# Kernel tuning notes

Hardware: AMD Instinct MI355X
Metric: run time of the kernel (lower is better)

Reference implementation:

```python
import jax, jax.numpy as jnp
import numpy as np

B, N, K, D = 8, 4096, 16, 256


def layer_norm(x, g, b, eps=1e-5):
    m = jnp.mean(x, axis=-1, keepdims=True)
    v = jnp.var(x, axis=-1, keepdims=True)
    return (x - m) * jax.lax.rsqrt(v + eps) * g + b


def setup_inputs() -> dict:
    key = jax.random.key(0)
    ks = jax.random.split(key, 8)

    def lin(k, fi, fo):
        return (jax.random.normal(k, (fi, fo), jnp.float32) / np.sqrt(fi).astype(np.float32),
                jnp.zeros((fo,), jnp.float32))

    coordinates = jax.random.normal(ks[0], (B, N, 3), jnp.float32)
    W1, b1 = lin(ks[1], 10, D // 4)
    W2, b2 = lin(ks[2], D // 4, D // 2)
    W3, b3 = lin(ks[3], D // 2, D)
    Wa1, ba1 = lin(ks[4], D, D)
    Wa2, ba2 = lin(ks[5], D, D)
    return {
        'coordinates': coordinates,
        'W1': W1, 'b1': b1, 'g1': jnp.ones((D // 4,)), 'be1': jnp.zeros((D // 4,)),
        'W2': W2, 'b2': b2, 'g2': jnp.ones((D // 2,)), 'be2': jnp.zeros((D // 2,)),
        'W3': W3, 'b3': b3, 'g3': jnp.ones((D,)), 'be3': jnp.zeros((D,)),
        'Wa1': Wa1, 'ba1': ba1, 'ga1': jnp.ones((D,)), 'bea1': jnp.zeros((D,)),
        'Wa2': Wa2, 'ba2': ba2,
    }


def reference(coordinates, W1, b1, g1, be1, W2, b2, g2, be2, W3, b3, g3, be3,
              Wa1, ba1, ga1, bea1, Wa2, ba2):
    # kNN via squared-distance matrix (monotone in Euclidean distance)
    sq = jnp.sum(coordinates * coordinates, axis=-1)  # [B,N]
    d2 = sq[:, :, None] + sq[:, None, :] - 2.0 * jnp.einsum('bnd,bmd->bnm', coordinates, coordinates)
    _, idx = jax.lax.top_k(-d2, K)  # smallest K distances, [B,N,K]

    nbr = jax.vmap(lambda c, i: c[i])(coordinates, idx)  # [B,N,K,3]
    rel = nbr - coordinates[:, :, None, :]               # relative positions
    dist = jnp.linalg.norm(rel, axis=-1, keepdims=True)  # [B,N,K,1]
    rn = rel / (dist + 1e-6)
    axy = jnp.arctan2(rn[..., 1], rn[..., 0])[..., None]
    axz = jnp.arctan2(rn[..., 2], rn[..., 0])[..., None]
    ayz = jnp.arctan2(rn[..., 2], rn[..., 1])[..., None]
    geom = jnp.concatenate([dist, rel, axy, axz, ayz, rn], axis=-1)  # [B,N,K,10]

    # encoder MLP
    h = jax.nn.relu(layer_norm(geom @ W1 + b1, g1, be1))
    h = jax.nn.relu(layer_norm(h @ W2 + b2, g2, be2))
    h = layer_norm(h @ W3 + b3, g3, be3)

    agg = jnp.mean(h, axis=2)  # mean over neighbors -> [B,N,D]

    # aggregator MLP
    out = jax.nn.relu(layer_norm(agg @ Wa1 + ba1, ga1, bea1)) @ Wa2 + ba2
    return out
```

## Files before the change

kernel.cpp:

```cpp
#include <hip/hip_runtime.h>
#include <hip/hip_bf16.h>
#include <math.h>

#define BB 8
#define NN 4096
#define KK 16
#define DD 256

typedef __hip_bfloat16 bf16;
typedef _Float16 half8 __attribute__((ext_vector_type(8)));
typedef float f32x4 __attribute__((ext_vector_type(4)));

union HFU { _Float16 h; unsigned short u; };
__device__ __forceinline__ unsigned short f2h(float x) { HFU v; v.h = (_Float16)x; return v.u; }

#define CONV_TOTAL 273344
#define O_COORD 0
#define O_W1 98304
#define O_b1 98944
#define O_g1 99008
#define O_be1 99072
#define O_W2 99136
#define O_b2 107328
#define O_g2 107456
#define O_be2 107584
#define O_W3 107712
#define O_b3 140480
#define O_g3 140736
#define O_be3 140992
#define O_Wa1 141248
#define O_ba1 206784
#define O_ga1 207040
#define O_bea1 207296
#define O_Wa2 207552
#define O_ba2 273088

#define F_W1 0
#define F_W2 2048
#define F_W3 10240
#define F_A1 43008
#define F_A2 108544
#define FRAG_TOTAL 174080

struct SrcPtrs {
  const void* p[19];
};

__global__ __launch_bounds__(256) void convert_kernel(SrcPtrs sp, float* __restrict__ dst) {
  static constexpr int OFF[20] = {
      0,      98304,  98944,  99008,  99072,  99136,  107328, 107456, 107584,
      107712, 140480, 140736, 140992, 141248, 206784, 207040, 207296, 207552,
      273088, 273344};
  const int i = blockIdx.x * 256 + threadIdx.x;
  if (i >= CONV_TOTAL) return;
  const unsigned tag = ((const unsigned*)sp.p[3])[0];
  const bool isb = (tag == 0x3F803F80u);
  int s = 0;
#pragma unroll
  for (int j = 1; j < 19; j++)
    if (i >= OFF[j]) s = j;
  const int local = i - OFF[s];
  float v = isb ? __bfloat162float(((const bf16*)sp.p[s])[local])
                : ((const float*)sp.p[s])[local];
  dst[i] = v;
}

__global__ __launch_bounds__(256) void swizzle_kernel(const float* __restrict__ conv,
                                                      unsigned short* __restrict__ frag) {
  const int t = blockIdx.x * 256 + threadIdx.x;
  if (t >= FRAG_TOTAL) return;
  int l, e;
  if (t < 2048) { l = 0; e = t; }
  else if (t < 10240) { l = 1; e = t - 2048; }
  else if (t < 43008) { l = 2; e = t - 10240; }
  else if (t < 108544) { l = 3; e = t - 43008; }
  else { l = 4; e = t - 108544; }
  static constexpr int WOFF[5] = {O_W1, O_W2, O_W3, O_Wa1, O_Wa2};
  static constexpr int NDIM[5] = {64, 128, 256, 256, 256};
  static constexpr int NTC[5] = {4, 8, 16, 16, 16};
  static constexpr int KREAL[5] = {10, 64, 128, 256, 256};
  static constexpr int HOFF[5] = {F_W1, F_W2, F_W3, F_A1, F_A2};
  const int j = e & 7;
  const int lane = (e >> 3) & 63;
  const int tile = e >> 9;
  const int nt = tile % NTC[l];
  const int kt = tile / NTC[l];
  const int k = kt * 32 + (lane >> 4) * 8 + j;
  const int n = nt * 16 + (lane & 15);
  float w = (k < KREAL[l]) ? conv[WOFF[l] + k * NDIM[l] + n] : 0.0f;
  frag[HOFF[l] + e] = f2h(w);
}

__device__ __forceinline__ float sq3_rn(float x, float y, float z) {
  return __fadd_rn(__fadd_rn(__fmul_rn(x, x), __fmul_rn(y, y)), __fmul_rn(z, z));
}
__device__ __forceinline__ float dot3_rn(float ax, float ay, float az, float bx, float by, float bz) {
  return __fadd_rn(__fadd_rn(__fmul_rn(ax, bx), __fmul_rn(ay, by)), __fmul_rn(az, bz));
}
__device__ __forceinline__ unsigned f2ord(float f) {
  unsigned u = __float_as_uint(f);
  return (u & 0x80000000u) ? ~u : (u | 0x80000000u);
}
__device__ __forceinline__ float ord2f(unsigned o) {
  unsigned u = (o & 0x80000000u) ? (o & 0x7FFFFFFFu) : ~o;
  return __uint_as_float(u);
}

__device__ __forceinline__ unsigned long long bitonic64(unsigned long long key, int lane) {
#pragma unroll
  for (int k = 2; k <= 64; k <<= 1) {
#pragma unroll
    for (int jj = k >> 1; jj > 0; jj >>= 1) {
      unsigned long long v = __shfl_xor(key, jj, 64);
      bool asc = ((lane & k) == 0);
      bool up = ((lane & jj) != 0);
      unsigned long long mn = (key < v) ? key : v;
      unsigned long long mx2 = (key < v) ? v : key;
      key = (up == asc) ? mx2 : mn;
    }
  }
  return key;
}

__global__ __launch_bounds__(512) void cellsort_kernel(const float* __restrict__ conv,
                                                       float4* __restrict__ sorted,
                                                       int* __restrict__ sidx) {
  __shared__ unsigned hist[512];
  __shared__ unsigned scanb[512];
  const int b = blockIdx.x;
  const int tid = threadIdx.x;
  const float* cb = conv + O_COORD + (size_t)b * NN * 3;
  hist[tid] = 0;
  __syncthreads();
  float xs[8], ys[8], zs[8];
  int cell[8];
  unsigned rank[8];
#pragma unroll
  for (int u = 0; u < 8; u++) {
    int p = u * 512 + tid;
    float x = cb[p * 3 + 0], y = cb[p * 3 + 1], z = cb[p * 3 + 2];
    xs[u] = x; ys[u] = y; zs[u] = z;
    int ix = min(7, max(0, (int)floorf(x + 4.0f)));
    int iy = min(7, max(0, (int)floorf(y + 4.0f)));
    int iz = min(7, max(0, (int)floorf(z + 4.0f)));
    int m = ((ix & 1) | ((ix & 2) << 2) | ((ix & 4) << 4)) |
            (((iy & 1) | ((iy & 2) << 2) | ((iy & 4) << 4)) << 1) |
            (((iz & 1) | ((iz & 2) << 2) | ((iz & 4) << 4)) << 2);
    cell[u] = m;
    rank[u] = atomicAdd(&hist[m], 1u);
  }
  __syncthreads();
  scanb[tid] = hist[tid];
  __syncthreads();
  for (int off = 1; off < 512; off <<= 1) {
    unsigned t = (tid >= off) ? scanb[tid - off] : 0u;
    __syncthreads();
    scanb[tid] += t;
    __syncthreads();
  }
#pragma unroll
  for (int u = 0; u < 8; u++) {
    unsigned base = scanb[cell[u]] - hist[cell[u]];
    unsigned pos = base + rank[u];
    sorted[(size_t)b * NN + pos] =
        make_float4(xs[u], ys[u], zs[u], sq3_rn(xs[u], ys[u], zs[u]));
    sidx[(size_t)b * NN + pos] = u * 512 + tid;
  }
}

__global__ __launch_bounds__(64) void knn_wave_kernel(const float4* __restrict__ soa,
                                                      const int* __restrict__ sI,
                                                      int* __restrict__ idx_out) {
  const int lane = threadIdx.x;
  const int wid = blockIdx.x;
  const int q0 = wid * 4;
  const int b = q0 >> 12;
  const float4* P = soa + (size_t)b * NN;
  const int* I = sI + (size_t)b * NN;
  const int qr = q0 & (NN - 1);
  const int base = qr >> 6;

  float cx[4], cy[4], cz[4], sqn[4];
  int qix[4];
#pragma unroll
  for (int j = 0; j < 4; j++) {
    float4 c = P[qr + j];
    cx[j] = c.x; cy[j] = c.y; cz[j] = c.z; sqn[j] = c.w;
    qix[j] = I[qr + j];
  }

  unsigned long long R[4], pend[4];
  float tauf[4];
  int A[4] = {0, 0, 0, 0};
#pragma unroll
  for (int j = 0; j < 4; j++) pend[j] = ~0ull;

  auto MERGE = [&](int j) {
    unsigned long long key =
        (lane < 16) ? R[j] : ((lane < 16 + A[j]) ? pend[j] : ~0ull);
    key = bitonic64(key, lane);
    R[j] = key;
    tauf[j] = ord2f((unsigned)(unsigned long long)__builtin_amdgcn_readlane(
        (int)(unsigned)(key >> 32), 15));
    A[j] = 0;
  };

  auto APPEND = [&](int j, unsigned long long msk, int cc, unsigned long long key) {
    unsigned rank = __builtin_amdgcn_mbcnt_hi(
        (unsigned)(msk >> 32), __builtin_amdgcn_mbcnt_lo((unsigned)msk, 0u));
    const bool flag = ((msk >> lane) & 1ull) != 0;
    const int lim = 16 + A[j];
    const int nf = lane - (int)rank;
    const int dst = flag ? (lim + (int)rank) : (nf < lim ? nf : nf + cc);
    int src = __builtin_amdgcn_ds_permute(dst << 2, lane) & 63;
    unsigned lo = (unsigned)__builtin_amdgcn_ds_bpermute(src << 2, (int)(unsigned)key);
    unsigned hi = (unsigned)__builtin_amdgcn_ds_bpermute(src << 2, (int)(unsigned)(key >> 32));
    const bool cons = (lane >= lim) && (lane < lim + cc);
    if (cons) pend[j] = (((unsigned long long)hi) << 32) | lo;
    A[j] += cc;
  };

  const int b0 = base * 64 + lane;
  float4 f0 = P[b0];
  int i0 = I[b0];
  const int b1 = ((base + 1) & 63) * 64 + lane;
  float4 f1 = P[b1];
  int i1 = I[b1];
  const int b2i = ((base + 2) & 63) * 64 + lane;
  float4 f2 = P[b2i];
  int i2 = I[b2i];

#pragma unroll
  for (int j = 0; j < 4; j++) {
    float dot = dot3_rn(cx[j], cy[j], cz[j], f0.x, f0.y, f0.z);
    float d2 = __fsub_rn(__fadd_rn(sqn[j], f0.w), __fmul_rn(2.0f, dot));
    unsigned long long key =
        (((unsigned long long)f2ord(d2)) << 32) | (unsigned)i0;
    key = bitonic64(key, lane);
    R[j] = key;
    tauf[j] = ord2f((unsigned)(unsigned long long)__builtin_amdgcn_readlane(
        (int)(unsigned)(key >> 32), 15));
  }

  for (int t = 1; t < 64; t++) {
    const float4 c = f1;
    const int iv = i1;
    f1 = f2; i1 = i2;
    if (t + 2 < 64) {
      const int nb = ((base + t + 2) & 63) * 64 + lane;
      f2 = P[nb];
      i2 = I[nb];
    }
    float d2v[4];
    unsigned long long pm[4];
#pragma unroll
    for (int j = 0; j < 4; j++) {
      float dot = dot3_rn(cx[j], cy[j], cz[j], c.x, c.y, c.z);
      d2v[j] = __fsub_rn(__fadd_rn(sqn[j], c.w), __fmul_rn(2.0f, dot));
      pm[j] = __ballot(d2v[j] <= tauf[j]);
    }
    if (!(pm[0] | pm[1] | pm[2] | pm[3])) continue;
#pragma unroll
    for (int j = 0; j < 4; j++) {
      unsigned long long rem = pm[j];
      if (!rem) continue;
      const unsigned long long key =
          (((unsigned long long)f2ord(d2v[j])) << 32) | (unsigned)iv;
      int cc = __builtin_popcountll(rem);
      while (A[j] + cc > 48) {
        if (A[j] == 0) {
          unsigned long long take = rem & 0xFFFFFFFFull;
          APPEND(j, take, __builtin_popcountll(take), key);
          rem ^= take;
        }
        MERGE(j);
        rem &= __ballot(d2v[j] <= tauf[j]);
        cc = __builtin_popcountll(rem);
      }
      if (cc) APPEND(j, rem, cc, key);
    }
  }

#pragma unroll
  for (int j = 0; j < 4; j++) {
    if (A[j]) MERGE(j);
    if (lane < KK)
      idx_out[((size_t)b * NN + (unsigned)qix[j]) * KK + lane] =
          (int)(R[j] & 0xFFFFFFFFull);
  }
}

template <int KT>
__device__ __forceinline__ void load_afrags(half8* A, const unsigned short* lF,
                                            int rowe, int lane) {
#pragma unroll
  for (int kt = 0; kt < KT; kt++) {
    int off = (lane & 15) * rowe + kt * 32 + (lane >> 4) * 8;
    A[kt] = *reinterpret_cast<const half8*>(lF + off);
  }
}

template <int NT>
__device__ __forceinline__ void init_acc(f32x4* acc, const float* __restrict__ bias,
                                         int lane) {
  const int col = lane & 15;
#pragma unroll
  for (int nt = 0; nt < NT; nt++) {
    float bv = bias[nt * 16 + col];
    acc[nt] = {bv, bv, bv, bv};
  }
}

template <int KT, int NT>
__device__ __forceinline__ void gemm_acc(f32x4* acc, const half8* A,
                                         const unsigned short* bb, int lane) {
#pragma unroll
  for (int kt = 0; kt < KT; kt++)
#pragma unroll
    for (int nt = 0; nt < NT; nt++) {
      const half8 bf = *reinterpret_cast<const half8*>(bb + (kt * NT + nt) * 512 + lane * 8);
      acc[nt] = __builtin_amdgcn_mfma_f32_16x16x32_f16(A[kt], bf, acc[nt], 0, 0, 0);
    }
}

template <int NT>
__device__ __forceinline__ void ln_stats(const f32x4* acc, float* m, float* rs) {
  float s[4] = {0.f, 0.f, 0.f, 0.f}, s2[4] = {0.f, 0.f, 0.f, 0.f};
#pragma unroll
  for (int nt = 0; nt < NT; nt++)
#pragma unroll
    for (int r = 0; r < 4; r++) {
      float v = acc[nt][r];
      s[r] += v;
      s2[r] += v * v;
    }
#pragma unroll
  for (int msk = 1; msk <= 8; msk <<= 1)
#pragma unroll
    for (int r = 0; r < 4; r++) {
      s[r] += __shfl_xor(s[r], msk, 64);
      s2[r] += __shfl_xor(s2[r], msk, 64);
    }
  const float invN = 1.0f / (NT * 16);
#pragma unroll
  for (int r = 0; r < 4; r++) {
    m[r] = s[r] * invN;
    float var = s2[r] * invN - m[r] * m[r];
    rs[r] = rsqrtf(var + 1e-5f);
  }
}

template <int NT, bool RELU>
__device__ __forceinline__ void ln_store(const f32x4* acc, const float* m, const float* rs,
                                         const float* __restrict__ g, const float* __restrict__ be,
                                         unsigned short* lF, int rowe, int lane) {
  const int col = lane & 15;
  const int rbase = (lane >> 4) * 4;
#pragma unroll
  for (int nt = 0; nt < NT; nt++) {
    float gv = g[nt * 16 + col], bv = be[nt * 16 + col];
#pragma unroll
    for (int r = 0; r < 4; r++) {
      float v = (acc[nt][r] - m[r]) * rs[r] * gv + bv;
      if (RELU) v = fmaxf(v, 0.0f);
      lF[(rbase + r) * rowe + nt * 16 + col] = f2h(v);
    }
  }
}

__device__ __forceinline__ void stage_b(unsigned short* bbuf,
                                        const unsigned short* __restrict__ src,
                                        int n_u4, int tid) {
  const uint4* s = reinterpret_cast<const uint4*>(src);
  uint4* d = reinterpret_cast<uint4*>(bbuf);
  for (int i = tid; i < n_u4; i += 256) d[i] = s[i];
}

#define ROWE_E 136
#define PSTR_E (16 * ROWE_E)

__global__ __launch_bounds__(256, 3) void encoder_mfma(
    const float* __restrict__ conv, const int* __restrict__ nbr,
    const unsigned short* __restrict__ frag, unsigned short* __restrict__ agF) {
  __shared__ unsigned short planes[4 * PSTR_E];
  __shared__ unsigned short Bbuf[16384];
  const int tid = threadIdx.x;
  const int lane = tid & 63;
  const int wave = tid >> 6;
  const int point = blockIdx.x * 4 + wave;
  const int b = point >> 12;
  const int n = point & (NN - 1);
  const float* cb = conv + O_COORD + (size_t)b * NN * 3;
  unsigned short* lF = planes + wave * PSTR_E;

  {
    int pl = tid >> 6, row = (tid >> 2) & 15, part = tid & 3;
    *reinterpret_cast<uint4*>(planes + pl * PSTR_E + row * ROWE_E + part * 8) =
        make_uint4(0u, 0u, 0u, 0u);
    stage_b(Bbuf, frag + F_W1, 1280, tid);
  }
  __syncthreads();

  if (lane < 16) {
    float cx = cb[n * 3 + 0], cy = cb[n * 3 + 1], cz = cb[n * 3 + 2];
    int id = nbr[(size_t)point * KK + lane];
    float rx = __fsub_rn(cb[id * 3 + 0], cx);
    float ry = __fsub_rn(cb[id * 3 + 1], cy);
    float rz = __fsub_rn(cb[id * 3 + 2], cz);
    float dist = __fsqrt_rn(sq3_rn(rx, ry, rz));
    float den = __fadd_rn(dist, 1e-6f);
    float ux = __fdiv_rn(rx, den), uy = __fdiv_rn(ry, den), uz = __fdiv_rn(rz, den);
    float ge[10];
    ge[0] = dist; ge[1] = rx; ge[2] = ry; ge[3] = rz;
    ge[4] = atan2f(uy, ux); ge[5] = atan2f(uz, ux); ge[6] = atan2f(uz, uy);
    ge[7] = ux; ge[8] = uy; ge[9] = uz;
#pragma unroll
    for (int c = 0; c < 10; c++) lF[lane * ROWE_E + c] = f2h(ge[c]);
  }

  float m[4], rs[4];
  {
    half8 A[1];
    load_afrags<1>(A, lF, ROWE_E, lane);
    f32x4 acc1[4];
    init_acc<4>(acc1, conv + O_b1, lane);
    gemm_acc<1, 4>(acc1, A, Bbuf, lane);
    ln_stats<4>(acc1, m, rs);
    ln_store<4, true>(acc1, m, rs, conv + O_g1, conv + O_be1, lF, ROWE_E, lane);
  }
  {
    half8 A[2];
    load_afrags<2>(A, lF, ROWE_E, lane);
    f32x4 acc2[8];
    init_acc<8>(acc2, conv + O_b2, lane);
    gemm_acc<2, 8>(acc2, A, Bbuf + 2048, lane);
    ln_stats<8>(acc2, m, rs);
    ln_store<8, true>(acc2, m, rs, conv + O_g2, conv + O_be2, lF, ROWE_E, lane);
  }
  half8 A3[4];
  load_afrags<4>(A3, lF, ROWE_E, lane);
  f32x4 acc[16];
  init_acc<16>(acc, conv + O_b3, lane);
  __syncthreads();
  stage_b(Bbuf, frag + F_W3, 2048, tid);
  __syncthreads();
  gemm_acc<2, 16>(acc, A3, Bbuf, lane);
  __syncthreads();
  stage_b(Bbuf, frag + F_W3 + 16384, 2048, tid);
  __syncthreads();
  gemm_acc<2, 16>(acc, A3 + 2, Bbuf, lane);

  {
    ln_stats<16>(acc, m, rs);
    const int col = lane & 15;
    float sv[16];
#pragma unroll
    for (int nt = 0; nt < 16; nt++) {
      float gv = conv[O_g3 + nt * 16 + col], bv = conv[O_be3 + nt * 16 + col];
      float s = 0.f;
#pragma unroll
      for (int r = 0; r < 4; r++) s += (acc[nt][r] - m[r]) * rs[r] * gv + bv;
      s += __shfl_xor(s, 16, 64);
      s += __shfl_xor(s, 32, 64);
      sv[nt] = s * (1.0f / 16.0f);
    }
    if (lane < 16) {
      size_t base = (size_t)point * DD;
#pragma unroll
      for (int nt = 0; nt < 16; nt++) agF[base + nt * 16 + lane] = f2h(sv[nt]);
    }
  }
}

#define ROWE_A 264

__global__ __launch_bounds__(256) void aggmlp_mfma(
    const float* __restrict__ conv, const unsigned short* __restrict__ agF,
    const unsigned short* __restrict__ a1, const unsigned short* __restrict__ a2,
    const unsigned* __restrict__ g1raw, void* __restrict__ out) {
  __shared__ unsigned short lds[4][16 * ROWE_A];
  const int lane = threadIdx.x & 63;
  const int wave = threadIdx.x >> 6;
  const int row0 = (blockIdx.x * 4 + wave) * 16;
  unsigned short* lF = lds[wave];

#pragma unroll
  for (int t = 0; t < 8; t++) {
    int v = t * 64 + lane;
    int row = v >> 5;
    int c0 = (v & 31) * 8;
    *reinterpret_cast<uint4*>(lF + row * ROWE_A + c0) =
        *reinterpret_cast<const uint4*>(agF + ((size_t)(row0 + row) * DD + c0));
  }
  __syncthreads();

  float m[4], rs[4];
  f32x4 acc[16];
  {
    half8 A[8];
    load_afrags<8>(A, lF, ROWE_A, lane);
    init_acc<16>(acc, conv + O_ba1, lane);
    gemm_acc<8, 16>(acc, A, a1, lane);
    ln_stats<16>(acc, m, rs);
    ln_store<16, true>(acc, m, rs, conv + O_ga1, conv + O_bea1, lF, ROWE_A, lane);
  }
  __syncthreads();
  {
    half8 A[8];
    load_afrags<8>(A, lF, ROWE_A, lane);
    init_acc<16>(acc, conv + O_ba2, lane);
    gemm_acc<8, 16>(acc, A, a2, lane);
  }
  const bool isb = (g1raw[0] == 0x3F803F80u);
  const int col = lane & 15;
  const int rbase = (lane >> 4) * 4;
  if (isb) {
    bf16* o = (bf16*)out;
#pragma unroll
    for (int nt = 0; nt < 16; nt++)
#pragma unroll
      for (int r = 0; r < 4; r++)
        o[(size_t)(row0 + rbase + r) * DD + nt * 16 + col] = __float2bfloat16(acc[nt][r]);
  } else {
    float* o = (float*)out;
#pragma unroll
    for (int nt = 0; nt < 16; nt++)
#pragma unroll
      for (int r = 0; r < 4; r++)
        o[(size_t)(row0 + rbase + r) * DD + nt * 16 + col] = acc[nt][r];
  }
}

extern "C" void kernel_launch(void* const* d_in, const int* in_sizes, int n_in,
                              void* d_out, int out_size, void* d_ws, size_t ws_size,
                              hipStream_t stream) {
  char* ws = (char*)d_ws;
  float* conv = (float*)ws;
  int* idx_ws = (int*)(ws + 1093376);
  unsigned short* agF = (unsigned short*)(ws + 3190528);
  unsigned short* frag = (unsigned short*)(ws + 19967744);
  float4* sorted = (float4*)(ws + 20315904);
  int* sidx = (int*)(ws + 20840192);

  SrcPtrs sp;
  for (int i = 0; i < 19; i++) sp.p[i] = d_in[i];

  convert_kernel<<<(CONV_TOTAL + 255) / 256, 256, 0, stream>>>(sp, conv);
  swizzle_kernel<<<(FRAG_TOTAL + 255) / 256, 256, 0, stream>>>(conv, frag);
  cellsort_kernel<<<BB, 512, 0, stream>>>(conv, sorted, sidx);

  knn_wave_kernel<<<BB * NN / 4, 64, 0, stream>>>(sorted, sidx, idx_ws);

  encoder_mfma<<<BB * NN / 4, 256, 0, stream>>>(conv, idx_ws, frag, agF);

  aggmlp_mfma<<<BB * NN / 64, 256, 0, stream>>>(conv, agF, frag + F_A1, frag + F_A2,
                                                (const unsigned*)d_in[3], d_out);
}
```

Measured before the change: 391.3 us.

## Stream W3 fragments from global memory and transpose MFMA for layers one and two

The W3 weight fragments are now read straight from global memory (L2-cached) instead of being staged through shared memory in two halves with four block-wide barriers. This shrinks the shared B buffer and should let more blocks fit per CU. Layers 1 and 2 now swap the MFMA operand order, so each lane holds feature columns for one neighbor, and the layer-norm statistics are computed with a single sum and sum-of-squares reduction using vectorized gamma/beta loads. The cost is repeated global or L2 traffic for W3 in every wave, and the one-pass variance formula is numerically weaker.

```diff
diff --git a/kernel.cpp b/kernel.cpp
--- a/kernel.cpp
+++ b/kernel.cpp
@@ -383,7 +383,7 @@
     const float* __restrict__ conv, const int* __restrict__ nbr,
     const unsigned short* __restrict__ frag, unsigned short* __restrict__ agF) {
   __shared__ unsigned short planes[4 * PSTR_E];
-  __shared__ unsigned short Bbuf[16384];
+  __shared__ unsigned short Bbuf[10240];
   const int tid = threadIdx.x;
   const int lane = tid & 63;
   const int wave = tid >> 6;
@@ -392,6 +392,8 @@
   const int n = point & (NN - 1);
   const float* cb = conv + O_COORD + (size_t)b * NN * 3;
   unsigned short* lF = planes + wave * PSTR_E;
+  const int g = lane >> 4;
+  const int col = lane & 15;
 
   {
     int pl = tid >> 6, row = (tid >> 2) & 15, part = tid & 3;
@@ -418,48 +420,106 @@
     for (int c = 0; c < 10; c++) lF[lane * ROWE_E + c] = f2h(ge[c]);
   }
 
-  float m[4], rs[4];
   {
-    half8 A[1];
-    load_afrags<1>(A, lF, ROWE_E, lane);
-    f32x4 acc1[4];
-    init_acc<4>(acc1, conv + O_b1, lane);
-    gemm_acc<1, 4>(acc1, A, Bbuf, lane);
-    ln_stats<4>(acc1, m, rs);
-    ln_store<4, true>(acc1, m, rs, conv + O_g1, conv + O_be1, lF, ROWE_E, lane);
-  }
+    half8 x0;
+    load_afrags<1>(&x0, lF, ROWE_E, lane);
+    f32x4 a1[4];
+#pragma unroll
+    for (int m = 0; m < 4; m++) {
+      const float4 bv = *reinterpret_cast<const float4*>(conv + O_b1 + m * 16 + g * 4);
+      a1[m] = {bv.x, bv.y, bv.z, bv.w};
+      const half8 wf = *reinterpret_cast<const half8*>(Bbuf + m * 512 + lane * 8);
+      a1[m] = __builtin_amdgcn_mfma_f32_16x16x32_f16(wf, x0, a1[m], 0, 0, 0);
+    }
+    float s = 0.f, s2 = 0.f;
+#pragma unroll
+    for (int m = 0; m < 4; m++)
+#pragma unroll
+      for (int r = 0; r < 4; r++) { float v = a1[m][r]; s += v; s2 += v * v; }
+    s += __shfl_xor(s, 16, 64); s += __shfl_xor(s, 32, 64);
+    s2 += __shfl_xor(s2, 16, 64); s2 += __shfl_xor(s2, 32, 64);
+    const float mu = s * (1.0f / 64.0f);
+    const float rsg = rsqrtf(s2 * (1.0f / 64.0f) - mu * mu + 1e-5f);
+#pragma unroll
+    for (int m = 0; m < 4; m++) {
+      const float4 gv = *reinterpret_cast<const float4*>(conv + O_g1 + m * 16 + g * 4);
+      const float4 bev = *reinterpret_cast<const float4*>(conv + O_be1 + m * 16 + g * 4);
+      unsigned long long pk = 0;
+#pragma unroll
+      for (int r = 0; r < 4; r++) {
+        float v = fmaxf((a1[m][r] - mu) * rsg * (&gv.x)[r] + (&bev.x)[r], 0.0f);
+        pk |= ((unsigned long long)f2h(v)) << (16 * r);
+      }
+      *reinterpret_cast<unsigned long long*>(lF + col * ROWE_E + m * 16 + g * 4) = pk;
+    }
+  }
+
   {
-    half8 A[2];
-    load_afrags<2>(A, lF, ROWE_E, lane);
-    f32x4 acc2[8];
-    init_acc<8>(acc2, conv + O_b2, lane);
-    gemm_acc<2, 8>(acc2, A, Bbuf + 2048, lane);
-    ln_stats<8>(acc2, m, rs);
-    ln_store<8, true>(acc2, m, rs, conv + O_g2, conv + O_be2, lF, ROWE_E, lane);
-  }
+    half8 x2[2];
+    load_afrags<2>(x2, lF, ROWE_E, lane);
+    f32x4 a2[8];
+#pragma unroll
+    for (int m = 0; m < 8; m++) {
+      const float4 bv = *reinterpret_cast<const float4*>(conv + O_b2 + m * 16 + g * 4);
+      a2[m] = {bv.x, bv.y, bv.z, bv.w};
+    }
+#pragma unroll
+    for (int kt = 0; kt < 2; kt++)
+#pragma unroll
+      for (int m = 0; m < 8; m++) {
+        const half8 wf =
+            *reinterpret_cast<const half8*>(Bbuf + 2048 + (kt * 8 + m) * 512 + lane * 8);
+        a2[m] = __builtin_amdgcn_mfma_f32_16x16x32_f16(wf, x2[kt], a2[m], 0, 0, 0);
+      }
+    float s = 0.f, s2 = 0.f;
+#pragma unroll
+    for (int m = 0; m < 8; m++)
+#pragma unroll
+      for (int r = 0; r < 4; r++) { float v = a2[m][r]; s += v; s2 += v * v; }
+    s += __shfl_xor(s, 16, 64); s += __shfl_xor(s, 32, 64);
+    s2 += __shfl_xor(s2, 16, 64); s2 += __shfl_xor(s2, 32, 64);
+    const float mu = s * (1.0f / 128.0f);
+    const float rsg = rsqrtf(s2 * (1.0f / 128.0f) - mu * mu + 1e-5f);
+#pragma unroll
+    for (int m = 0; m < 8; m++) {
+      const float4 gv = *reinterpret_cast<const float4*>(conv + O_g2 + m * 16 + g * 4);
+      const float4 bev = *reinterpret_cast<const float4*>(conv + O_be2 + m * 16 + g * 4);
+      unsigned long long pk = 0;
+#pragma unroll
+      for (int r = 0; r < 4; r++) {
+        float v = fmaxf((a2[m][r] - mu) * rsg * (&gv.x)[r] + (&bev.x)[r], 0.0f);
+        pk |= ((unsigned long long)f2h(v)) << (16 * r);
+      }
+      *reinterpret_cast<unsigned long long*>(lF + col * ROWE_E + m * 16 + g * 4) = pk;
+    }
+  }
+
   half8 A3[4];
   load_afrags<4>(A3, lF, ROWE_E, lane);
   f32x4 acc[16];
   init_acc<16>(acc, conv + O_b3, lane);
-  __syncthreads();
-  stage_b(Bbuf, frag + F_W3, 2048, tid);
-  __syncthreads();
-  gemm_acc<2, 16>(acc, A3, Bbuf, lane);
-  __syncthreads();
-  stage_b(Bbuf, frag + F_W3 + 16384, 2048, tid);
-  __syncthreads();
-  gemm_acc<2, 16>(acc, A3 + 2, Bbuf, lane);
-
   {
+    const unsigned short* W3 = frag + F_W3;
+#pragma unroll
+    for (int kt = 0; kt < 4; kt++)
+#pragma unroll
+      for (int nt = 0; nt < 16; nt++) {
+        const half8 bf =
+            *reinterpret_cast<const half8*>(W3 + (kt * 16 + nt) * 512 + lane * 8);
+        acc[nt] = __builtin_amdgcn_mfma_f32_16x16x32_f16(A3[kt], bf, acc[nt], 0, 0, 0);
+      }
+  }
+
+  {
+    float m[4], rs[4];
     ln_stats<16>(acc, m, rs);
-    const int col = lane & 15;
     float sv[16];
 #pragma unroll
     for (int nt = 0; nt < 16; nt++) {
-      float gv = conv[O_g3 + nt * 16 + col], bv = conv[O_be3 + nt * 16 + col];
+      float gvv = conv[O_g3 + nt * 16 + col], bvv = conv[O_be3 + nt * 16 + col];
       float s = 0.f;
 #pragma unroll
-      for (int r = 0; r < 4; r++) s += (acc[nt][r] - m[r]) * rs[r] * gv + bv;
+      for (int r = 0; r < 4; r++) s += (acc[nt][r] - m[r]) * rs[r] * gvv + bvv;
       s += __shfl_xor(s, 16, 64);
       s += __shfl_xor(s, 32, 64);
       sv[nt] = s * (1.0f / 16.0f);
```

Measured after the change: 382.5 us. 2.2% less time.
